# Kernel optimization log

Measured on AMD Instinct MI355X. Metric: run time of the kernel, lower is better.

Reference implementation:

```python
import jax, jax.numpy as jnp
import numpy as np

N = 50000      # nodes
F_IN = 128     # num_feat
HID = 128      # hidden size
OUT = 47       # num_out (classes)
E = 600000     # graph edges
EGO_E = 1200000  # concatenated egonet edges


def _linear_params(key, fan_in, fan_out):
    s = 1.0 / np.sqrt(fan_in)
    kw, kb = jax.random.split(key)
    W = jax.random.uniform(kw, (fan_in, fan_out), jnp.float32, -s, s)
    b = jax.random.uniform(kb, (fan_out,), jnp.float32, -s, s)
    return W, b


def setup_inputs() -> dict:
    key = jax.random.key(0)
    ks = jax.random.split(key, 8)
    x_in = jax.random.normal(ks[0], (N, F_IN), jnp.float32)
    edge_index_in = jax.random.randint(ks[1], (2, E), 0, N)
    ego_edge_index = jax.random.randint(ks[2], (2, EGO_E), 0, N)
    W_ego0, b_ego0 = _linear_params(ks[3], F_IN, F_IN)
    W_gin0, b_gin0 = _linear_params(ks[4], F_IN, HID)
    W_ego1, b_ego1 = _linear_params(ks[5], HID, HID)
    W_gin1, b_gin1 = _linear_params(ks[6], HID, OUT)
    return {
        "x_in": x_in, "edge_index_in": edge_index_in, "ego_edge_index": ego_edge_index,
        "W_ego0": W_ego0, "b_ego0": b_ego0, "W_gin0": W_gin0, "b_gin0": b_gin0,
        "W_ego1": W_ego1, "b_ego1": b_ego1, "W_gin1": W_gin1, "b_gin1": b_gin1,
    }


def reference(x_in, edge_index_in, ego_edge_index,
              W_ego0, b_ego0, W_gin0, b_gin0,
              W_ego1, b_ego1, W_gin1, b_gin1):
    n = x_in.shape[0]
    ego_row, ego_col = ego_edge_index[0], ego_edge_index[1]
    src, tgt = edge_index_in[0], edge_index_in[1]

    def do_conv(x):
        # sum_i spmm(A_i, x) == scatter-add over concatenated egonet edges, then / N
        return jax.ops.segment_sum(x[ego_col], ego_row, num_segments=n) * (1.0 / n)

    def gin(x, W, b):
        # GINConv(nn=Linear), eps=0: Linear(x + sum_{j->i} x_j)
        aggr = jax.ops.segment_sum(x[src], tgt, num_segments=n)
        return (x + aggr) @ W + b

    # layer 0: ['Ego','GIN', relu_mid=True, relu_end=True]
    x = do_conv(x_in) @ W_ego0 + b_ego0
    x = jax.nn.relu(x)
    x = gin(x, W_gin0, b_gin0)
    x = jax.nn.relu(x)
    # layer 1: ['Ego','GIN', relu_mid=True, relu_end=False]
    x = do_conv(x) @ W_ego1 + b_ego1
    x = jax.nn.relu(x)
    x = gin(x, W_gin1, b_gin1)
    return jax.nn.log_softmax(x, axis=1)
```

## Files before the change

kernel.cpp:

```cpp
#include <hip/hip_runtime.h>

#define SCAP_EGO 8192
#define SCAP_E   4096

typedef unsigned short ushort_t;
typedef unsigned int uint_t;
typedef __attribute__((ext_vector_type(8))) short bf16x8;
typedef __attribute__((ext_vector_type(4))) float f32x4;

__device__ inline float lo16(uint_t u) { return __uint_as_float(u << 16); }
__device__ inline float hi16(uint_t u) { return __uint_as_float(u & 0xFFFF0000u); }
__device__ inline ushort_t f2bf(float f) {
    uint_t i = __float_as_uint(f);
    return (ushort_t)((i + 0x7FFFu + ((i >> 16) & 1u)) >> 16);
}
__device__ inline uint_t pack2(float a, float b) {
    return (uint_t)f2bf(a) | ((uint_t)f2bf(b) << 16);
}
union U8 { uint4 u; bf16x8 v; };

__global__ __launch_bounds__(256) void cvt_zero(
    const float* __restrict__ x, ushort_t* __restrict__ xb, int n8,
    int* __restrict__ z, int nz4)
{
    int i = blockIdx.x * 256 + threadIdx.x;
    if (i < n8) {
        const float4* p = (const float4*)(x + (size_t)i * 8);
        float4 a = p[0], b = p[1];
        uint4 o;
        o.x = pack2(a.x, a.y); o.y = pack2(a.z, a.w);
        o.z = pack2(b.x, b.y); o.w = pack2(b.z, b.w);
        *(uint4*)(xb + (size_t)i * 8) = o;
    }
    if (i < nz4) ((int4*)z)[i] = make_int4(0, 0, 0, 0);
}

__global__ __launch_bounds__(256) void cvt_weights(
    const float* __restrict__ W0, const float* __restrict__ W1,
    const float* __restrict__ W2, const float* __restrict__ W3,
    ushort_t* __restrict__ T0, ushort_t* __restrict__ T1,
    ushort_t* __restrict__ T2, ushort_t* __restrict__ T3)
{
    int gid = blockIdx.x * 256 + threadIdx.x;
    if (gid < 49152) {
        int mi = gid >> 14;
        int r = gid & 16383;
        int n = r >> 7, k = r & 127;
        const float* W = mi == 0 ? W0 : (mi == 1 ? W1 : W2);
        ushort_t* T = mi == 0 ? T0 : (mi == 1 ? T1 : T2);
        T[n * 128 + k] = f2bf(W[k * 128 + n]);
    } else if (gid < 49152 + 6144) {
        int r = gid - 49152;
        int n = r >> 7, k = r & 127;
        T3[n * 128 + k] = (n < 47) ? f2bf(W3[k * 47 + n]) : (ushort_t)0;
    }
}

__global__ __launch_bounds__(256) void bin_edges(
    const int* __restrict__ dst, const int* __restrict__ src, int nE, int scap,
    int* __restrict__ bincur, int2* __restrict__ stage)
{
    __shared__ int bcnt[256];
    __shared__ int gbase[256];
    int t = threadIdx.x;
    bcnt[t] = 0;
    __syncthreads();
    int base = blockIdx.x * 4096;
    int d[16], s[16], l[16];
#pragma unroll
    for (int i = 0; i < 16; i++) {
        int e = base + t + i * 256;
        if (e < nE) {
            d[i] = dst[e]; s[i] = src[e];
            l[i] = atomicAdd(&bcnt[d[i] >> 8], 1);
        } else d[i] = -1;
    }
    __syncthreads();
    if (bcnt[t]) gbase[t] = atomicAdd(&bincur[t], bcnt[t]);
    __syncthreads();
#pragma unroll
    for (int i = 0; i < 16; i++) {
        if (d[i] >= 0) {
            int b = d[i] >> 8;
            int slot = gbase[b] + l[i];
            if (slot < scap) stage[(size_t)b * scap + slot] = make_int2(d[i], s[i]);
        }
    }
}

__global__ __launch_bounds__(256) void build_csr(
    const int* __restrict__ bincur, const int2* __restrict__ stage, int scap,
    int* __restrict__ cnt, int* __restrict__ rowptr, int* __restrict__ packed,
    int nNodes)
{
    __shared__ int sc[256];
    __shared__ int wcur[256];
    int b = blockIdx.x, t = threadIdx.x;
    int m = bincur[b]; if (m > scap) m = scap;
    const int2* st = stage + (size_t)b * scap;
    sc[t] = 0;
    __syncthreads();
    for (int e = t; e < m; e += 256) atomicAdd(&sc[st[e].x & 255], 1);
    __syncthreads();
    int v = sc[t];
    __syncthreads();
    sc[t] = v;
    __syncthreads();
    for (int off = 1; off < 256; off <<= 1) {
        int y = (t >= off) ? sc[t - off] : 0;
        __syncthreads();
        sc[t] += y;
        __syncthreads();
    }
    int excl = sc[t] - v;
    int node = b * 256 + t;
    if (node < nNodes) { cnt[node] = v; rowptr[node] = b * scap + excl; }
    wcur[t] = excl;
    __syncthreads();
    int* pk = packed + (size_t)b * scap;
    for (int e = t; e < m; e += 256) {
        int2 p = st[e];
        int slot = atomicAdd(&wcur[p.x & 255], 1);
        pk[slot] = p.y;
    }
}

__global__ __launch_bounds__(256) void gather_bf(
    const ushort_t* __restrict__ x, const int* __restrict__ cnt,
    const int* __restrict__ rowptr, const int* __restrict__ packed,
    ushort_t* __restrict__ outb, int nNodes, float scale, int selfAdd)
{
    int wave = threadIdx.x >> 6, lane = threadIdx.x & 63;
    int n = blockIdx.x * 4 + wave;
    if (n >= nNodes) return;
    int len = cnt[n];
    const int* row = packed + rowptr[n];
    const ushort_t* base = x + lane * 2;
    float ax = 0.f, ay = 0.f;
    int e = 0;
    for (; e + 3 < len; e += 4) {
        uint_t w0 = *(const uint_t*)(base + (size_t)row[e + 0] * 128);
        uint_t w1 = *(const uint_t*)(base + (size_t)row[e + 1] * 128);
        uint_t w2 = *(const uint_t*)(base + (size_t)row[e + 2] * 128);
        uint_t w3 = *(const uint_t*)(base + (size_t)row[e + 3] * 128);
        ax += lo16(w0) + lo16(w1) + lo16(w2) + lo16(w3);
        ay += hi16(w0) + hi16(w1) + hi16(w2) + hi16(w3);
    }
    for (; e < len; e++) {
        uint_t w = *(const uint_t*)(base + (size_t)row[e] * 128);
        ax += lo16(w); ay += hi16(w);
    }
    if (selfAdd) {
        uint_t w = *(const uint_t*)(base + (size_t)n * 128);
        ax += lo16(w); ay += hi16(w);
    }
    *(uint_t*)(outb + (size_t)n * 128 + lane * 2) = pack2(ax * scale, ay * scale);
}

template<int NCOLT, bool RELU>
__global__ __launch_bounds__(256) void gemm_mfma(
    const ushort_t* __restrict__ A, const ushort_t* __restrict__ WT,
    const float* __restrict__ bias, ushort_t* __restrict__ outb,
    int nrows, int ncols)
{
    __shared__ ushort_t Ws[NCOLT * 16][136];
    int t = threadIdx.x;
    for (int j = t; j < NCOLT * 16 * 16; j += 256) {
        int n = j >> 4, kq = (j & 15) << 3;
        *(uint4*)&Ws[n][kq] = *(const uint4*)(WT + n * 128 + kq);
    }
    int wave = t >> 6, lane = t & 63;
    int m = lane & 15, quad = lane >> 4;
    int rowBase = blockIdx.x * 64 + wave * 16;
    int arow = rowBase + m; if (arow >= nrows) arow = 0;
    bf16x8 afr[4];
#pragma unroll
    for (int kt = 0; kt < 4; kt++) {
        U8 u; u.u = *(const uint4*)(A + (size_t)arow * 128 + kt * 32 + quad * 8);
        afr[kt] = u.v;
    }
    __syncthreads();
    f32x4 acc[NCOLT];
#pragma unroll
    for (int ct = 0; ct < NCOLT; ct++) acc[ct] = (f32x4){0.f, 0.f, 0.f, 0.f};
#pragma unroll
    for (int ct = 0; ct < NCOLT; ct++) {
#pragma unroll
        for (int kt = 0; kt < 4; kt++) {
            bf16x8 b = *(const bf16x8*)&Ws[ct * 16 + m][kt * 32 + quad * 8];
            acc[ct] = __builtin_amdgcn_mfma_f32_16x16x32_bf16(afr[kt], b, acc[ct], 0, 0, 0);
        }
    }
#pragma unroll
    for (int ct = 0; ct < NCOLT; ct++) {
        int col = ct * 16 + m;
        if (col >= ncols) continue;
        float bb = bias[col];
#pragma unroll
        for (int r = 0; r < 4; r++) {
            int row = rowBase + quad * 4 + r;
            if (row < nrows) {
                float v = acc[ct][r] + bb;
                if (RELU) v = fmaxf(v, 0.f);
                outb[(size_t)row * ncols + col] = f2bf(v);
            }
        }
    }
}

__global__ __launch_bounds__(256) void logsoftmax47_b(
    const ushort_t* __restrict__ logitsb, float* __restrict__ out, int nrows)
{
    int wave = threadIdx.x >> 6, lane = threadIdx.x & 63;
    int row = blockIdx.x * 4 + wave;
    if (row >= nrows) return;
    float v = -INFINITY;
    if (lane < 47) v = __uint_as_float(((uint_t)logitsb[(size_t)row * 47 + lane]) << 16);
    float m = v;
#pragma unroll
    for (int off = 32; off; off >>= 1) m = fmaxf(m, __shfl_xor(m, off, 64));
    float e = (lane < 47) ? __expf(v - m) : 0.f;
    float s = e;
#pragma unroll
    for (int off = 32; off; off >>= 1) s += __shfl_xor(s, off, 64);
    float r = v - m - __logf(s);
    if (lane < 47) out[(size_t)row * 47 + lane] = r;
}

extern "C" void kernel_launch(void* const* d_in, const int* in_sizes, int n_in,
                              void* d_out, int out_size, void* d_ws, size_t ws_size,
                              hipStream_t stream) {
    const float* x_in   = (const float*)d_in[0];
    const int*   edge   = (const int*)d_in[1];
    const int*   ego    = (const int*)d_in[2];
    const float* W_ego0 = (const float*)d_in[3];
    const float* b_ego0 = (const float*)d_in[4];
    const float* W_gin0 = (const float*)d_in[5];
    const float* b_gin0 = (const float*)d_in[6];
    const float* W_ego1 = (const float*)d_in[7];
    const float* b_ego1 = (const float*)d_in[8];
    const float* W_gin1 = (const float*)d_in[9];
    const float* b_gin1 = (const float*)d_in[10];
    float* out = (float*)d_out;

    const int N     = in_sizes[0] / 128;
    const int E     = in_sizes[1] / 2;
    const int EGO_E = in_sizes[2] / 2;
    const float invN = 1.0f / (float)N;
    const int NB    = (N + 255) >> 8;

    const size_t NBELEM = (size_t)N * 128;
    ushort_t* Xb = (ushort_t*)d_ws;
    ushort_t* G  = Xb + NBELEM;
    ushort_t* H  = G + NBELEM;
    ushort_t* Lg = H + NBELEM;
    ushort_t* T0 = Lg + ((size_t)N * 47 + 7) / 8 * 8;
    ushort_t* T1 = T0 + 16384;
    ushort_t* T2 = T1 + 16384;
    ushort_t* T3 = T2 + 16384;
    int* ip = (int*)(T3 + 6144);
    int* cnt_ego  = ip;              ip += N;
    int* rp_ego   = ip;              ip += N;
    int* cnt_edge = ip;              ip += N;
    int* rp_edge  = ip;              ip += N;
    int* bincur   = ip;              ip += 512;
    int2* stage_ego  = (int2*)ip;    ip += (size_t)NB * SCAP_EGO * 2;
    int*  pk_ego     = ip;           ip += (size_t)NB * SCAP_EGO;
    int2* stage_edge = (int2*)ip;    ip += (size_t)NB * SCAP_E * 2;
    int*  pk_edge    = ip;           ip += (size_t)NB * SCAP_E;

    const int gGemm = (N + 63) / 64;
    const int gNode = (N + 3) / 4;
    const int gBinE = (EGO_E + 4095) / 4096;
    const int gBinF = (E + 4095) / 4096;
    const int gCvt  = ((N * 128 / 8) + 255) / 256;

    cvt_zero<<<gCvt, 256, 0, stream>>>(x_in, Xb, N * 128 / 8, bincur, 128);
    cvt_weights<<<217, 256, 0, stream>>>(W_ego0, W_gin0, W_ego1, W_gin1, T0, T1, T2, T3);
    bin_edges<<<gBinE, 256, 0, stream>>>(ego, ego + EGO_E, EGO_E, SCAP_EGO, bincur, stage_ego);
    bin_edges<<<gBinF, 256, 0, stream>>>(edge + E, edge, E, SCAP_E, bincur + 256, stage_edge);
    build_csr<<<NB, 256, 0, stream>>>(bincur, stage_ego, SCAP_EGO, cnt_ego, rp_ego, pk_ego, N);
    build_csr<<<NB, 256, 0, stream>>>(bincur + 256, stage_edge, SCAP_E, cnt_edge, rp_edge, pk_edge, N);

    gather_bf<<<gNode, 256, 0, stream>>>(Xb, cnt_ego, rp_ego, pk_ego, G, N, invN, 0);
    gemm_mfma<8, true><<<gGemm, 256, 0, stream>>>(G, T0, b_ego0, H, N, 128);
    gather_bf<<<gNode, 256, 0, stream>>>(H, cnt_edge, rp_edge, pk_edge, G, N, 1.f, 1);
    gemm_mfma<8, true><<<gGemm, 256, 0, stream>>>(G, T1, b_gin0, H, N, 128);
    gather_bf<<<gNode, 256, 0, stream>>>(H, cnt_ego, rp_ego, pk_ego, G, N, invN, 0);
    gemm_mfma<8, true><<<gGemm, 256, 0, stream>>>(G, T2, b_ego1, H, N, 128);
    gather_bf<<<gNode, 256, 0, stream>>>(H, cnt_edge, rp_edge, pk_edge, G, N, 1.f, 1);
    gemm_mfma<3, false><<<gGemm, 256, 0, stream>>>(G, T3, b_gin1, Lg, N, 47);
    logsoftmax47_b<<<gNode, 256, 0, stream>>>(Lg, out, N);
}
```

Measured before the change: 375.3 us.

## Fuse final GEMM with log-softmax, merge prep kernels, widen gather loads

Merges the input and weight conversion kernels into one prep launch. The gather kernel now assigns 32 lanes per node, each loading 8 bytes, so every block handles 8 nodes. The last 47-column GEMM is fused with log-softmax using in-register shuffles across the 16-lane column group, which removes the bf16 logits buffer and one launch. The fused path also skips rounding the logits to bf16 before the softmax, which slightly changes precision.

```diff
diff --git a/kernel.cpp b/kernel.cpp
--- a/kernel.cpp
+++ b/kernel.cpp
@@ -19,11 +19,16 @@
 }
 union U8 { uint4 u; bf16x8 v; };
 
-__global__ __launch_bounds__(256) void cvt_zero(
+__global__ __launch_bounds__(256) void prep(
     const float* __restrict__ x, ushort_t* __restrict__ xb, int n8,
-    int* __restrict__ z, int nz4)
+    const float* __restrict__ W0, const float* __restrict__ W1,
+    const float* __restrict__ W2, const float* __restrict__ W3,
+    ushort_t* __restrict__ T0, ushort_t* __restrict__ T1,
+    ushort_t* __restrict__ T2, ushort_t* __restrict__ T3,
+    int* __restrict__ z)
 {
     int i = blockIdx.x * 256 + threadIdx.x;
+    if (i < 128) ((int4*)z)[i] = make_int4(0, 0, 0, 0);
     if (i < n8) {
         const float4* p = (const float4*)(x + (size_t)i * 8);
         float4 a = p[0], b = p[1];
@@ -32,25 +37,15 @@
         o.z = pack2(b.x, b.y); o.w = pack2(b.z, b.w);
         *(uint4*)(xb + (size_t)i * 8) = o;
     }
-    if (i < nz4) ((int4*)z)[i] = make_int4(0, 0, 0, 0);
-}
-
-__global__ __launch_bounds__(256) void cvt_weights(
-    const float* __restrict__ W0, const float* __restrict__ W1,
-    const float* __restrict__ W2, const float* __restrict__ W3,
-    ushort_t* __restrict__ T0, ushort_t* __restrict__ T1,
-    ushort_t* __restrict__ T2, ushort_t* __restrict__ T3)
-{
-    int gid = blockIdx.x * 256 + threadIdx.x;
-    if (gid < 49152) {
-        int mi = gid >> 14;
-        int r = gid & 16383;
+    if (i < 49152) {
+        int mi = i >> 14;
+        int r = i & 16383;
         int n = r >> 7, k = r & 127;
         const float* W = mi == 0 ? W0 : (mi == 1 ? W1 : W2);
         ushort_t* T = mi == 0 ? T0 : (mi == 1 ? T1 : T2);
         T[n * 128 + k] = f2bf(W[k * 128 + n]);
-    } else if (gid < 49152 + 6144) {
-        int r = gid - 49152;
+    } else if (i < 49152 + 6144) {
+        int r = i - 49152;
         int n = r >> 7, k = r & 127;
         T3[n * 128 + k] = (n < 47) ? f2bf(W3[k * 47 + n]) : (ushort_t)0;
     }
@@ -130,42 +125,47 @@
     const int* __restrict__ rowptr, const int* __restrict__ packed,
     ushort_t* __restrict__ outb, int nNodes, float scale, int selfAdd)
 {
-    int wave = threadIdx.x >> 6, lane = threadIdx.x & 63;
-    int n = blockIdx.x * 4 + wave;
+    int g = threadIdx.x >> 5, lane = threadIdx.x & 31;
+    int n = blockIdx.x * 8 + g;
     if (n >= nNodes) return;
     int len = cnt[n];
     const int* row = packed + rowptr[n];
-    const ushort_t* base = x + lane * 2;
-    float ax = 0.f, ay = 0.f;
+    const ushort_t* base = x + lane * 4;
+    float a0 = 0.f, a1 = 0.f, a2 = 0.f, a3 = 0.f;
     int e = 0;
     for (; e + 3 < len; e += 4) {
-        uint_t w0 = *(const uint_t*)(base + (size_t)row[e + 0] * 128);
-        uint_t w1 = *(const uint_t*)(base + (size_t)row[e + 1] * 128);
-        uint_t w2 = *(const uint_t*)(base + (size_t)row[e + 2] * 128);
-        uint_t w3 = *(const uint_t*)(base + (size_t)row[e + 3] * 128);
-        ax += lo16(w0) + lo16(w1) + lo16(w2) + lo16(w3);
-        ay += hi16(w0) + hi16(w1) + hi16(w2) + hi16(w3);
+        int s0 = row[e], s1 = row[e + 1], s2 = row[e + 2], s3 = row[e + 3];
+        uint2 w0 = *(const uint2*)(base + (size_t)s0 * 128);
+        uint2 w1 = *(const uint2*)(base + (size_t)s1 * 128);
+        uint2 w2 = *(const uint2*)(base + (size_t)s2 * 128);
+        uint2 w3 = *(const uint2*)(base + (size_t)s3 * 128);
+        a0 += lo16(w0.x) + lo16(w1.x) + lo16(w2.x) + lo16(w3.x);
+        a1 += hi16(w0.x) + hi16(w1.x) + hi16(w2.x) + hi16(w3.x);
+        a2 += lo16(w0.y) + lo16(w1.y) + lo16(w2.y) + lo16(w3.y);
+        a3 += hi16(w0.y) + hi16(w1.y) + hi16(w2.y) + hi16(w3.y);
     }
     for (; e < len; e++) {
-        uint_t w = *(const uint_t*)(base + (size_t)row[e] * 128);
-        ax += lo16(w); ay += hi16(w);
+        uint2 w = *(const uint2*)(base + (size_t)row[e] * 128);
+        a0 += lo16(w.x); a1 += hi16(w.x); a2 += lo16(w.y); a3 += hi16(w.y);
     }
     if (selfAdd) {
-        uint_t w = *(const uint_t*)(base + (size_t)n * 128);
-        ax += lo16(w); ay += hi16(w);
-    }
-    *(uint_t*)(outb + (size_t)n * 128 + lane * 2) = pack2(ax * scale, ay * scale);
-}
-
-template<int NCOLT, bool RELU>
+        uint2 w = *(const uint2*)(base + (size_t)n * 128);
+        a0 += lo16(w.x); a1 += hi16(w.x); a2 += lo16(w.y); a3 += hi16(w.y);
+    }
+    uint2 o;
+    o.x = pack2(a0 * scale, a1 * scale);
+    o.y = pack2(a2 * scale, a3 * scale);
+    *(uint2*)(outb + (size_t)n * 128 + lane * 4) = o;
+}
+
+template<bool RELU>
 __global__ __launch_bounds__(256) void gemm_mfma(
     const ushort_t* __restrict__ A, const ushort_t* __restrict__ WT,
-    const float* __restrict__ bias, ushort_t* __restrict__ outb,
-    int nrows, int ncols)
-{
-    __shared__ ushort_t Ws[NCOLT * 16][136];
+    const float* __restrict__ bias, ushort_t* __restrict__ outb, int nrows)
+{
+    __shared__ ushort_t Ws[128][136];
     int t = threadIdx.x;
-    for (int j = t; j < NCOLT * 16 * 16; j += 256) {
+    for (int j = t; j < 128 * 16; j += 256) {
         int n = j >> 4, kq = (j & 15) << 3;
         *(uint4*)&Ws[n][kq] = *(const uint4*)(WT + n * 128 + kq);
     }
@@ -180,11 +180,11 @@
         afr[kt] = u.v;
     }
     __syncthreads();
-    f32x4 acc[NCOLT];
-#pragma unroll
-    for (int ct = 0; ct < NCOLT; ct++) acc[ct] = (f32x4){0.f, 0.f, 0.f, 0.f};
-#pragma unroll
-    for (int ct = 0; ct < NCOLT; ct++) {
+    f32x4 acc[8];
+#pragma unroll
+    for (int ct = 0; ct < 8; ct++) acc[ct] = (f32x4){0.f, 0.f, 0.f, 0.f};
+#pragma unroll
+    for (int ct = 0; ct < 8; ct++) {
 #pragma unroll
         for (int kt = 0; kt < 4; kt++) {
             bf16x8 b = *(const bf16x8*)&Ws[ct * 16 + m][kt * 32 + quad * 8];
@@ -192,9 +192,8 @@
         }
     }
 #pragma unroll
-    for (int ct = 0; ct < NCOLT; ct++) {
+    for (int ct = 0; ct < 8; ct++) {
         int col = ct * 16 + m;
-        if (col >= ncols) continue;
         float bb = bias[col];
 #pragma unroll
         for (int r = 0; r < 4; r++) {
@@ -202,29 +201,67 @@
             if (row < nrows) {
                 float v = acc[ct][r] + bb;
                 if (RELU) v = fmaxf(v, 0.f);
-                outb[(size_t)row * ncols + col] = f2bf(v);
+                outb[(size_t)row * 128 + col] = f2bf(v);
             }
         }
     }
 }
 
-__global__ __launch_bounds__(256) void logsoftmax47_b(
-    const ushort_t* __restrict__ logitsb, float* __restrict__ out, int nrows)
-{
-    int wave = threadIdx.x >> 6, lane = threadIdx.x & 63;
-    int row = blockIdx.x * 4 + wave;
-    if (row >= nrows) return;
-    float v = -INFINITY;
-    if (lane < 47) v = __uint_as_float(((uint_t)logitsb[(size_t)row * 47 + lane]) << 16);
-    float m = v;
-#pragma unroll
-    for (int off = 32; off; off >>= 1) m = fmaxf(m, __shfl_xor(m, off, 64));
-    float e = (lane < 47) ? __expf(v - m) : 0.f;
-    float s = e;
-#pragma unroll
-    for (int off = 32; off; off >>= 1) s += __shfl_xor(s, off, 64);
-    float r = v - m - __logf(s);
-    if (lane < 47) out[(size_t)row * 47 + lane] = r;
+__global__ __launch_bounds__(256) void gemm47_lsm(
+    const ushort_t* __restrict__ A, const ushort_t* __restrict__ WT,
+    const float* __restrict__ bias, float* __restrict__ out, int nrows)
+{
+    __shared__ ushort_t Ws[48][136];
+    int t = threadIdx.x;
+    for (int j = t; j < 48 * 16; j += 256) {
+        int n = j >> 4, kq = (j & 15) << 3;
+        *(uint4*)&Ws[n][kq] = *(const uint4*)(WT + n * 128 + kq);
+    }
+    int wave = t >> 6, lane = t & 63;
+    int m = lane & 15, quad = lane >> 4;
+    int rowBase = blockIdx.x * 64 + wave * 16;
+    int arow = rowBase + m; if (arow >= nrows) arow = 0;
+    bf16x8 afr[4];
+#pragma unroll
+    for (int kt = 0; kt < 4; kt++) {
+        U8 u; u.u = *(const uint4*)(A + (size_t)arow * 128 + kt * 32 + quad * 8);
+        afr[kt] = u.v;
+    }
+    __syncthreads();
+    f32x4 acc[3];
+#pragma unroll
+    for (int ct = 0; ct < 3; ct++) acc[ct] = (f32x4){0.f, 0.f, 0.f, 0.f};
+#pragma unroll
+    for (int ct = 0; ct < 3; ct++) {
+#pragma unroll
+        for (int kt = 0; kt < 4; kt++) {
+            bf16x8 b = *(const bf16x8*)&Ws[ct * 16 + m][kt * 32 + quad * 8];
+            acc[ct] = __builtin_amdgcn_mfma_f32_16x16x32_bf16(afr[kt], b, acc[ct], 0, 0, 0);
+        }
+    }
+    int c0 = m, c1 = 16 + m, c2 = 32 + m;
+    bool has2 = (c2 < 47);
+    float b0 = bias[c0], b1 = bias[c1], b2 = has2 ? bias[c2] : 0.f;
+#pragma unroll
+    for (int r = 0; r < 4; r++) {
+        int row = rowBase + quad * 4 + r;
+        float v0 = acc[0][r] + b0;
+        float v1 = acc[1][r] + b1;
+        float v2 = has2 ? (acc[2][r] + b2) : -INFINITY;
+        float mx = fmaxf(fmaxf(v0, v1), v2);
+#pragma unroll
+        for (int off = 8; off; off >>= 1) mx = fmaxf(mx, __shfl_xor(mx, off, 64));
+        float s = __expf(v0 - mx) + __expf(v1 - mx) + (has2 ? __expf(v2 - mx) : 0.f);
+#pragma unroll
+        for (int off = 8; off; off >>= 1) s += __shfl_xor(s, off, 64);
+        float lse = mx + __logf(s);
+        if (row < nrows) {
+            float* o = out + (size_t)row * 47;
+            o[c0] = v0 - lse;
+            o[c1] = v1 - lse;
+            if (has2) o[c2] = v2 - lse;
+        }
+    }
 }
 
 extern "C" void kernel_launch(void* const* d_in, const int* in_sizes, int n_in,
@@ -253,8 +290,7 @@
     ushort_t* Xb = (ushort_t*)d_ws;
     ushort_t* G  = Xb + NBELEM;
     ushort_t* H  = G + NBELEM;
-    ushort_t* Lg = H + NBELEM;
-    ushort_t* T0 = Lg + ((size_t)N * 47 + 7) / 8 * 8;
+    ushort_t* T0 = H + NBELEM;
     ushort_t* T1 = T0 + 16384;
     ushort_t* T2 = T1 + 16384;
     ushort_t* T3 = T2 + 16384;
@@ -269,26 +305,26 @@
     int2* stage_edge = (int2*)ip;    ip += (size_t)NB * SCAP_E * 2;
     int*  pk_edge    = ip;           ip += (size_t)NB * SCAP_E;
 
-    const int gGemm = (N + 63) / 64;
-    const int gNode = (N + 3) / 4;
-    const int gBinE = (EGO_E + 4095) / 4096;
-    const int gBinF = (E + 4095) / 4096;
-    const int gCvt  = ((N * 128 / 8) + 255) / 256;
-
-    cvt_zero<<<gCvt, 256, 0, stream>>>(x_in, Xb, N * 128 / 8, bincur, 128);
-    cvt_weights<<<217, 256, 0, stream>>>(W_ego0, W_gin0, W_ego1, W_gin1, T0, T1, T2, T3);
+    const int gGemm  = (N + 63) / 64;
+    const int gNode8 = (N + 7) / 8;
+    const int gBinE  = (EGO_E + 4095) / 4096;
+    const int gBinF  = (E + 4095) / 4096;
+    const int gCvt   = ((N * 128 / 8) + 255) / 256;
+
+    prep<<<gCvt, 256, 0, stream>>>(x_in, Xb, N * 128 / 8,
+                                   W_ego0, W_gin0, W_ego1, W_gin1,
+                                   T0, T1, T2, T3, bincur);
     bin_edges<<<gBinE, 256, 0, stream>>>(ego, ego + EGO_E, EGO_E, SCAP_EGO, bincur, stage_ego);
     bin_edges<<<gBinF, 256, 0, stream>>>(edge + E, edge, E, SCAP_E, bincur + 256, stage_edge);
     build_csr<<<NB, 256, 0, stream>>>(bincur, stage_ego, SCAP_EGO, cnt_ego, rp_ego, pk_ego, N);
     build_csr<<<NB, 256, 0, stream>>>(bincur + 256, stage_edge, SCAP_E, cnt_edge, rp_edge, pk_edge, N);
 
-    gather_bf<<<gNode, 256, 0, stream>>>(Xb, cnt_ego, rp_ego, pk_ego, G, N, invN, 0);
-    gemm_mfma<8, true><<<gGemm, 256, 0, stream>>>(G, T0, b_ego0, H, N, 128);
-    gather_bf<<<gNode, 256, 0, stream>>>(H, cnt_edge, rp_edge, pk_edge, G, N, 1.f, 1);
-    gemm_mfma<8, true><<<gGemm, 256, 0, stream>>>(G, T1, b_gin0, H, N, 128);
-    gather_bf<<<gNode, 256, 0, stream>>>(H, cnt_ego, rp_ego, pk_ego, G, N, invN, 0);
-    gemm_mfma<8, true><<<gGemm, 256, 0, stream>>>(G, T2, b_ego1, H, N, 128);
-    gather_bf<<<gNode, 256, 0, stream>>>(H, cnt_edge, rp_edge, pk_edge, G, N, 1.f, 1);
-    gemm_mfma<3, false><<<gGemm, 256, 0, stream>>>(G, T3, b_gin1, Lg, N, 47);
-    logsoftmax47_b<<<gNode, 256, 0, stream>>>(Lg, out, N);
-}
+    gather_bf<<<gNode8, 256, 0, stream>>>(Xb, cnt_ego, rp_ego, pk_ego, G, N, invN, 0);
+    gemm_mfma<true><<<gGemm, 256, 0, stream>>>(G, T0, b_ego0, H, N);
+    gather_bf<<<gNode8, 256, 0, stream>>>(H, cnt_edge, rp_edge, pk_edge, G, N, 1.f, 1);
+    gemm_mfma<true><<<gGemm, 256, 0, stream>>>(G, T1, b_gin0, H, N);
+    gather_bf<<<gNode8, 256, 0, stream>>>(H, cnt_ego, rp_ego, pk_ego, G, N, invN, 0);
+    gemm_mfma<true><<<gGemm, 256, 0, stream>>>(G, T2, b_ego1, H, N);
+    gather_bf<<<gNode8, 256, 0, stream>>>(H, cnt_edge, rp_edge, pk_edge, G, N, 1.f, 1);
+    gemm47_lsm<<<gGemm, 256, 0, stream>>>(G, T3, b_gin1, out, N);
+}
```

Measured after the change: 338.0 us. 1.11x faster.
